# Kernel tuning notes

Hardware: AMD Instinct MI355X
Metric: run time of the kernel (lower is better)

Reference implementation:

```python
import jax, jax.numpy as jnp
import numpy as np

B, C, T, H, W = 8, 128, 16, 32, 32
M, N, CS = 64, 64, 64


def setup_inputs() -> dict:
    key = jax.random.key(0)
    ks = jax.random.split(key, 12)
    s = 0.02
    return {
        "input": jax.random.normal(ks[0], (B, C, T, H, W), dtype=jnp.float32),
        "condition": jax.random.normal(ks[1], (B, CS), dtype=jnp.float32),
        # 1x1x1 Conv3d weights collapse to (out, in) matrices
        "W_phi": jax.random.normal(ks[2], (M, C), dtype=jnp.float32) * s,
        "b_phi": jax.random.normal(ks[3], (M,), dtype=jnp.float32) * s,
        "W_theta": jax.random.normal(ks[4], (N, C), dtype=jnp.float32) * s,
        "b_theta": jax.random.normal(ks[5], (N,), dtype=jnp.float32) * s,
        "W_rho": jax.random.normal(ks[6], (N, C), dtype=jnp.float32) * s,
        "b_rho": jax.random.normal(ks[7], (N,), dtype=jnp.float32) * s,
        "W1": jax.random.normal(ks[8], (CS, CS), dtype=jnp.float32) * s,
        "b1": jax.random.normal(ks[9], (CS,), dtype=jnp.float32) * s,
        "W2": jax.random.normal(ks[10], (H * W, CS), dtype=jnp.float32) * s,
        "b2": jax.random.normal(ks[11], (H * W,), dtype=jnp.float32) * s,
    }


def _pointwise_conv3d(x, Wt, b):
    # Conv3d with kernel=1, stride=1 == channel mixing
    return jnp.einsum('bcthw,oc->bothw', x, Wt) + b[None, :, None, None, None]


def reference(input, condition, W_phi, b_phi, W_theta, b_theta, W_rho, b_rho, W1, b1, W2, b2):
    x = input.reshape(-1, C, T, H, W)
    cond = condition.reshape(x.shape[0], -1)
    A = _pointwise_conv3d(x, W_phi, b_phi)                       # (b,m,t,h,w)
    B0 = _pointwise_conv3d(x, W_theta, b_theta)                  # (b,n,t,h,w)
    Bm = jax.nn.softmax(B0.reshape(B0.shape[0], B0.shape[1], -1), axis=-1).reshape(B0.shape)
    # FC_Cond: Linear+ReLU, Linear+ReLU, then softmax over h*w
    h1 = jax.nn.relu(cond @ W1.T + b1)
    h2 = jax.nn.relu(h1 @ W2.T + b2)
    Cm = jax.nn.softmax(h2, axis=-1).reshape(-1, H, W)           # (b,h,w)
    BC = Bm * Cm[:, None, None, :, :]                            # (b,n,t,h,w)
    AB_T = jnp.einsum('bmthw,bnthw->bmn', A, BC)                 # (b,m,n)
    V = jax.nn.softmax(_pointwise_conv3d(x, W_rho, b_rho), axis=1)
    Z = jnp.einsum('bmn,bnthw->bmthw', AB_T, V)
    attn = jnp.transpose(Bm * V, (0, 1, 3, 4, 2))                # (b,n,h,w,t)
    return (Z, attn)
```

## Files before the change

### kernel.cpp

```cpp
#include <hip/hip_runtime.h>

#define CC 128
#define SB 16384

typedef _Float16 half4_t __attribute__((ext_vector_type(4)));
typedef _Float16 half8_t __attribute__((ext_vector_type(8)));
typedef float    f32x4  __attribute__((ext_vector_type(4)));

#define WH_OFF   0u
#define ABH_OFF  0u
#define BIAS_OFF 49152u
#define CM_OFF   50176u
#define SUME_OFF 82944u
#define XT_OFF   262144u
#define VT_OFF   33816576u

__global__ void k0_setup(const float* __restrict__ cond,
                         const float* __restrict__ W_phi, const float* __restrict__ b_phi,
                         const float* __restrict__ W_theta, const float* __restrict__ b_theta,
                         const float* __restrict__ W_rho, const float* __restrict__ b_rho,
                         const float* __restrict__ W1, const float* __restrict__ b1,
                         const float* __restrict__ W2, const float* __restrict__ b2,
                         char* __restrict__ wsc) {
  __shared__ float sc[64], sh1[64], red[256];
  int t = threadIdx.x, bid = blockIdx.x;
  if (bid < 8) {
    int b = bid;
    if (t < 64) sc[t] = cond[b*64 + t];
    __syncthreads();
    if (t < 64) {
      float acc = b1[t];
      for (int k = 0; k < 64; ++k) acc += sc[k] * W1[t*64 + k];
      sh1[t] = fmaxf(acc, 0.f);
    }
    __syncthreads();
    float ev[4]; float ps = 0.f;
    #pragma unroll
    for (int q = 0; q < 4; ++q) {
      int o = q*256 + t;
      float acc = b2[o];
      for (int k = 0; k < 64; ++k) acc += sh1[k] * W2[o*64 + k];
      ev[q] = __expf(fmaxf(acc, 0.f));
      ps += ev[q];
    }
    red[t] = ps; __syncthreads();
    for (int s = 128; s > 0; s >>= 1) { if (t < s) red[t] += red[t+s]; __syncthreads(); }
    float inv = 1.f / red[0];
    float* cm = (float*)(wsc + CM_OFF);
    #pragma unroll
    for (int q = 0; q < 4; ++q) cm[b*1024 + q*256 + t] = ev[q] * inv;
  } else {
    int r = bid - 8;
    _Float16* wh = (_Float16*)(wsc + WH_OFF);
    for (int i = r*256 + t; i < 24576; i += 2048) {
      int set = i >> 13, mk = i & 8191;
      const float* W = (set == 0) ? W_phi : (set == 1 ? W_theta : W_rho);
      wh[i] = (_Float16)W[mk];
    }
    if (r == 0 && t < 192) {
      float* bias = (float*)(wsc + BIAS_OFF);
      bias[t] = (t < 64) ? b_phi[t] : (t < 128 ? b_theta[t-64] : b_rho[t-128]);
    }
    if (r == 1) {
      float* se = (float*)(wsc + SUME_OFF);
      for (int i = t; i < 512; i += 256) se[i] = 0.f;
    }
  }
}

__global__ __launch_bounds__(256, 2) void kT_transpose(const float* __restrict__ x,
                                                       _Float16* __restrict__ xt) {
  __shared__ float Xs[128*133];
  int t = threadIdx.x, bid = blockIdx.x;
  int b = bid >> 7, chunk = bid & 127;
  int s0 = chunk * 128;
  const float* xb = x + (size_t)b*CC*SB + s0;
  #pragma unroll
  for (int r = 0; r < 16; ++r) {
    int fid = r*256 + t;
    int c = fid >> 5, s4 = (fid & 31) << 2;
    *(float4*)&Xs[c*133 + s4] = *(const float4*)(xb + (size_t)c*SB + s4);
  }
  __syncthreads();
  int c8 = t & 15, sl = t >> 4;
  _Float16* xo = xt + ((size_t)b*SB + s0)*128 + c8*8;
  #pragma unroll
  for (int it = 0; it < 8; ++it) {
    int s = it*16 + sl;
    half8_t h;
    #pragma unroll
    for (int i = 0; i < 8; ++i) h[i] = (_Float16)Xs[(c8*8 + i)*133 + s];
    *(half8_t*)(xo + (size_t)s*128) = h;
  }
}

__global__ __launch_bounds__(256, 2) void kC_main(
    const _Float16* __restrict__ xt, const _Float16* __restrict__ wh,
    const float* __restrict__ bias, const float* __restrict__ cm,
    float* __restrict__ sumE, _Float16* __restrict__ vt,
    char* __restrict__ ptb,
    float* __restrict__ part) {
  __shared__ _Float16 Xt_l[128*136];
  __shared__ _Float16 A_l[64*136];
  __shared__ _Float16 E_l[64*136];
  __shared__ float se_l[256];

  int t = threadIdx.x;
  int lane = t & 63, wv = t >> 6, ln = lane & 15, q = lane >> 4;
  int bid = blockIdx.x, b = bid >> 7, chunk = bid & 127;
  int s0 = chunk * 128;

  #pragma unroll
  for (int r = 0; r < 8; ++r) {
    int fid = r*256 + t;
    int s = fid >> 4, c16 = fid & 15;
    *(half8_t*)&Xt_l[s*136 + c16*8] =
        *(const half8_t*)(xt + ((size_t)b*SB + s0 + s)*128 + c16*8);
  }
  __syncthreads();

  half8_t bf[2][4];
  int myp = wv * 32;
  #pragma unroll
  for (int nt = 0; nt < 2; ++nt)
    #pragma unroll
    for (int kk = 0; kk < 4; ++kk)
      bf[nt][kk] = *(half8_t*)&Xt_l[(myp + nt*16 + ln)*136 + kk*32 + q*8];

  int gsl[2] = { s0 + myp + ln, s0 + myp + 16 + ln };
  float cmv[2] = { cm[b*1024 + (gsl[0] & 1023)], cm[b*1024 + (gsl[1] & 1023)] };

  half8_t af[4][4];
  f32x4 d[4][2];
  float ev[4][2][4];

  auto conv = [&](int setoff) {
    #pragma unroll
    for (int mt = 0; mt < 4; ++mt)
      #pragma unroll
      for (int kk = 0; kk < 4; ++kk)
        af[mt][kk] = *(const half8_t*)(wh + setoff + (mt*16 + ln)*128 + kk*32 + q*8);
    #pragma unroll
    for (int mt = 0; mt < 4; ++mt)
      #pragma unroll
      for (int nt = 0; nt < 2; ++nt)
        d[mt][nt] = (f32x4){0.f, 0.f, 0.f, 0.f};
    #pragma unroll
    for (int kk = 0; kk < 4; ++kk)
      #pragma unroll
      for (int mt = 0; mt < 4; ++mt)
        #pragma unroll
        for (int nt = 0; nt < 2; ++nt)
          d[mt][nt] = __builtin_amdgcn_mfma_f32_16x16x32_f16(af[mt][kk], bf[nt][kk],
                                                             d[mt][nt], 0, 0, 0);
  };

  conv(0);
  #pragma unroll
  for (int mt = 0; mt < 4; ++mt) {
    float bv[4]; *(float4*)bv = *(const float4*)(bias + mt*16 + q*4);
    #pragma unroll
    for (int nt = 0; nt < 2; ++nt)
      #pragma unroll
      for (int r = 0; r < 4; ++r)
        A_l[(mt*16 + q*4 + r)*136 + myp + nt*16 + ln] = (_Float16)(d[mt][nt][r] + bv[r]);
  }

  conv(8192);
  float sp[4][4];
  #pragma unroll
  for (int mt = 0; mt < 4; ++mt) {
    float bv[4]; *(float4*)bv = *(const float4*)(bias + 64 + mt*16 + q*4);
    #pragma unroll
    for (int r = 0; r < 4; ++r) {
      #pragma unroll
      for (int nt = 0; nt < 2; ++nt) {
        float e = __expf(d[mt][nt][r] + bv[r]);
        ev[mt][nt][r] = e;
        E_l[(mt*16 + q*4 + r)*136 + myp + nt*16 + ln] = (_Float16)(e * cmv[nt]);
      }
      sp[mt][r] = ev[mt][0][r] + ev[mt][1][r];
    }
  }
  #pragma unroll
  for (int mt = 0; mt < 4; ++mt)
    #pragma unroll
    for (int r = 0; r < 4; ++r) {
      float v = sp[mt][r];
      v += __shfl_xor(v, 1); v += __shfl_xor(v, 2);
      v += __shfl_xor(v, 4); v += __shfl_xor(v, 8);
      sp[mt][r] = v;
    }
  if (ln == 0) {
    #pragma unroll
    for (int mt = 0; mt < 4; ++mt)
      #pragma unroll
      for (int r = 0; r < 4; ++r)
        se_l[wv*64 + mt*16 + q*4 + r] = sp[mt][r];
  }

  conv(16384);
  #pragma unroll
  for (int mt = 0; mt < 4; ++mt) {
    float bv[4]; *(float4*)bv = *(const float4*)(bias + 128 + mt*16 + q*4);
    #pragma unroll
    for (int nt = 0; nt < 2; ++nt)
      #pragma unroll
      for (int r = 0; r < 4; ++r)
        d[mt][nt][r] = __expf(d[mt][nt][r] + bv[r]);
  }
  float cs[2] = {0.f, 0.f};
  #pragma unroll
  for (int mt = 0; mt < 4; ++mt)
    #pragma unroll
    for (int nt = 0; nt < 2; ++nt)
      #pragma unroll
      for (int r = 0; r < 4; ++r) cs[nt] += d[mt][nt][r];
  #pragma unroll
  for (int nt = 0; nt < 2; ++nt) {
    cs[nt] += __shfl_xor(cs[nt], 16);
    cs[nt] += __shfl_xor(cs[nt], 32);
    cs[nt] = 1.f / cs[nt];
  }
  #pragma unroll
  for (int nt = 0; nt < 2; ++nt) {
    size_t grow = (size_t)b*SB + gsl[nt];
    _Float16* vrow = vt + grow*64;
    char* prow = ptb + grow*256 + 128;
    #pragma unroll
    for (int mt = 0; mt < 4; ++mt) {
      half4_t hv, hp;
      #pragma unroll
      for (int r = 0; r < 4; ++r) {
        float vv = d[mt][nt][r] * cs[nt];
        hv[r] = (_Float16)vv;
        hp[r] = (_Float16)(vv * ev[mt][nt][r]);
      }
      *(half4_t*)(vrow + mt*16 + q*4) = hv;
      *(half4_t*)(prow + (size_t)(mt*16 + q*4)*2) = hp;
    }
  }
  __syncthreads();

  if (t < 64) {
    float ssum = se_l[t] + se_l[64+t] + se_l[128+t] + se_l[192+t];
    atomicAdd(&sumE[b*64 + t], ssum);
  }

  f32x4 dab[4];
  #pragma unroll
  for (int n2 = 0; n2 < 4; ++n2) dab[n2] = (f32x4){0.f, 0.f, 0.f, 0.f};
  #pragma unroll
  for (int kk = 0; kk < 4; ++kk) {
    half8_t aab = *(half8_t*)&A_l[(wv*16 + ln)*136 + kk*32 + q*8];
    #pragma unroll
    for (int n2 = 0; n2 < 4; ++n2) {
      half8_t bab = *(half8_t*)&E_l[(n2*16 + ln)*136 + kk*32 + q*8];
      dab[n2] = __builtin_amdgcn_mfma_f32_16x16x32_f16(aab, bab, dab[n2], 0, 0, 0);
    }
  }
  float* pp = part + (size_t)bid*4096;
  #pragma unroll
  for (int n2 = 0; n2 < 4; ++n2)
    #pragma unroll
    for (int r = 0; r < 4; ++r)
      pp[(wv*16 + q*4 + r)*64 + n2*16 + ln] = dab[n2][r];
}

__global__ void k2_reduce(const float* __restrict__ part, const float* __restrict__ sumE,
                          _Float16* __restrict__ abh) {
  int idx = blockIdx.x*256 + threadIdx.x;
  int b = idx >> 12, mn = idx & 4095, n = mn & 63;
  const float* p = part + (size_t)b*128*4096 + mn;
  float s = 0.f;
  #pragma unroll 4
  for (int k = 0; k < 128; ++k) s += p[(size_t)k*4096];
  abh[idx] = (_Float16)(s * (1024.f / sumE[b*64 + n]));
}

__global__ __launch_bounds__(256) void k3_z(const _Float16* __restrict__ abh,
                                            const _Float16* __restrict__ vt,
                                            float* __restrict__ zout) {
  __shared__ _Float16 Ah[64*72];
  int t = threadIdx.x;
  int lane = t & 63, wv = t >> 6, ln = lane & 15, q = lane >> 4;
  int bid = blockIdx.x, b = bid >> 6, chunk = bid & 63;
  int s0 = chunk * 256;
  #pragma unroll
  for (int r = 0; r < 2; ++r) {
    int fid = r*256 + t;
    int m = fid >> 3, n8 = fid & 7;
    *(half8_t*)&Ah[m*72 + n8*8] = *(const half8_t*)(abh + b*4096 + m*64 + n8*8);
  }
  __syncthreads();
  half8_t a8[4][2];
  #pragma unroll
  for (int mt = 0; mt < 4; ++mt)
    #pragma unroll
    for (int kk = 0; kk < 2; ++kk)
      a8[mt][kk] = *(half8_t*)&Ah[(mt*16 + ln)*72 + kk*32 + q*8];
  int sw = s0 + wv*64;
  #pragma unroll
  for (int nt = 0; nt < 4; ++nt) {
    int sb = sw + nt*16 + ln;
    const _Float16* vrow = vt + ((size_t)b*SB + sb)*64;
    half8_t b8[2];
    b8[0] = *(const half8_t*)(vrow + q*8);
    b8[1] = *(const half8_t*)(vrow + 32 + q*8);
    f32x4 dz[4];
    #pragma unroll
    for (int mt = 0; mt < 4; ++mt) dz[mt] = (f32x4){0.f, 0.f, 0.f, 0.f};
    #pragma unroll
    for (int kk = 0; kk < 2; ++kk)
      #pragma unroll
      for (int mt = 0; mt < 4; ++mt)
        dz[mt] = __builtin_amdgcn_mfma_f32_16x16x32_f16(a8[mt][kk], b8[kk], dz[mt], 0, 0, 0);
    #pragma unroll
    for (int mt = 0; mt < 4; ++mt)
      #pragma unroll
      for (int r = 0; r < 4; ++r)
        zout[((size_t)(b*64 + mt*16 + q*4 + r))*SB + sb] = dz[mt][r] * (1.f/1024.f);
  }
}

__global__ __launch_bounds__(256) void k4_attn(const char* __restrict__ ptb,
                                               const float* __restrict__ sumE,
                                               float* __restrict__ outA) {
  __shared__ _Float16 P_l[256*72];
  int t = threadIdx.x, bid = blockIdx.x;
  int b = bid >> 6, hw0 = (bid & 63) * 16;
  int st = t >> 4, h = t & 15;
  int s = st*1024 + hw0 + h;
  const char* prow = ptb + ((size_t)b*SB + s)*256 + 128;
  #pragma unroll
  for (int c8 = 0; c8 < 8; ++c8)
    *(half8_t*)&P_l[t*72 + c8*8] = *(const half8_t*)(prow + c8*16);
  __syncthreads();
  int n = t >> 2, oc = t & 3;
  float ri = 1.f / sumE[b*64 + n];
  float* orow = outA + 8388608 + (size_t)(b*64 + n)*SB + hw0*16;
  #pragma unroll
  for (int i = 0; i < 16; ++i) {
    int j = oc*64 + i*4;
    int hh = j >> 4, stb = j & 15;
    float w[4];
    #pragma unroll
    for (int r = 0; r < 4; ++r)
      w[r] = (float)P_l[((stb + r)*16 + hh)*72 + n] * ri;
    *(float4*)(orow + j) = *(float4*)w;
  }
}

extern "C" void kernel_launch(void* const* d_in, const int* in_sizes, int n_in,
                              void* d_out, int out_size, void* d_ws, size_t ws_size,
                              hipStream_t stream) {
  const float* input   = (const float*)d_in[0];
  const float* cond    = (const float*)d_in[1];
  const float* W_phi   = (const float*)d_in[2];
  const float* b_phi   = (const float*)d_in[3];
  const float* W_theta = (const float*)d_in[4];
  const float* b_theta = (const float*)d_in[5];
  const float* W_rho   = (const float*)d_in[6];
  const float* b_rho   = (const float*)d_in[7];
  const float* W1      = (const float*)d_in[8];
  const float* b1      = (const float*)d_in[9];
  const float* W2      = (const float*)d_in[10];
  const float* b2      = (const float*)d_in[11];
  char* wsc = (char*)d_ws;
  float* out = (float*)d_out;

  const _Float16* wh = (const _Float16*)(wsc + WH_OFF);
  _Float16* abh  = (_Float16*)(wsc + ABH_OFF);
  const float* bias = (const float*)(wsc + BIAS_OFF);
  const float* cmp  = (const float*)(wsc + CM_OFF);
  float* sumE  = (float*)(wsc + SUME_OFF);
  _Float16* xt = (_Float16*)(wsc + XT_OFF);
  _Float16* vt = (_Float16*)(wsc + VT_OFF);
  float* part  = out + 8388608;

  hipLaunchKernelGGL(k0_setup, dim3(16), dim3(256), 0, stream,
                     cond, W_phi, b_phi, W_theta, b_theta, W_rho, b_rho,
                     W1, b1, W2, b2, wsc);
  hipLaunchKernelGGL(kT_transpose, dim3(1024), dim3(256), 0, stream, input, xt);
  hipLaunchKernelGGL(kC_main, dim3(1024), dim3(256), 0, stream,
                     xt, wh, bias, cmp, sumE, vt, (char*)(wsc + XT_OFF), part);
  hipLaunchKernelGGL(k2_reduce, dim3(128), dim3(256), 0, stream, part, sumE, abh);
  hipLaunchKernelGGL(k3_z, dim3(512), dim3(256), 0, stream, abh, vt, out);
  hipLaunchKernelGGL(k4_attn, dim3(512), dim3(256), 0, stream,
                     (const char*)(wsc + XT_OFF), sumE, out);
}
```

Baseline: 227.1 us.

## Fuse input transpose into main kernel and merge Z/attn kernels

Removes the separate fp32-to-fp16 transpose kernel. The main kernel now loads the channel-major input directly, converts it to fp16 in shared memory, and gathers the MFMA B fragments with strided LDS reads. Shared memory is aliased and the occupancy hint is raised to 4 blocks per CU. The P buffer is compacted to 128 bytes per row, k3 and k4 are merged into one launch split by block index, and k2 uses 128-thread blocks. This saves a full global round trip of the input and two launches, at the cost of scalar strided LDS gathers and possible bank conflicts.

```diff
diff --git a/kernel.cpp b/kernel.cpp
--- a/kernel.cpp
+++ b/kernel.cpp
@@ -3,6 +3,7 @@
 #define CC 128
 #define SB 16384
 
+typedef _Float16 half2_t __attribute__((ext_vector_type(2)));
 typedef _Float16 half4_t __attribute__((ext_vector_type(4)));
 typedef _Float16 half8_t __attribute__((ext_vector_type(8)));
 typedef float    f32x4  __attribute__((ext_vector_type(4)));
@@ -12,7 +13,7 @@
 #define BIAS_OFF 49152u
 #define CM_OFF   50176u
 #define SUME_OFF 82944u
-#define XT_OFF   262144u
+#define PT_OFF   262144u
 #define VT_OFF   33816576u
 
 __global__ void k0_setup(const float* __restrict__ cond,
@@ -68,67 +69,53 @@
   }
 }
 
-__global__ __launch_bounds__(256, 2) void kT_transpose(const float* __restrict__ x,
-                                                       _Float16* __restrict__ xt) {
-  __shared__ float Xs[128*133];
-  int t = threadIdx.x, bid = blockIdx.x;
-  int b = bid >> 7, chunk = bid & 127;
-  int s0 = chunk * 128;
-  const float* xb = x + (size_t)b*CC*SB + s0;
-  #pragma unroll
-  for (int r = 0; r < 16; ++r) {
-    int fid = r*256 + t;
-    int c = fid >> 5, s4 = (fid & 31) << 2;
-    *(float4*)&Xs[c*133 + s4] = *(const float4*)(xb + (size_t)c*SB + s4);
-  }
-  __syncthreads();
-  int c8 = t & 15, sl = t >> 4;
-  _Float16* xo = xt + ((size_t)b*SB + s0)*128 + c8*8;
-  #pragma unroll
-  for (int it = 0; it < 8; ++it) {
-    int s = it*16 + sl;
-    half8_t h;
-    #pragma unroll
-    for (int i = 0; i < 8; ++i) h[i] = (_Float16)Xs[(c8*8 + i)*133 + s];
-    *(half8_t*)(xo + (size_t)s*128) = h;
-  }
-}
-
-__global__ __launch_bounds__(256, 2) void kC_main(
-    const _Float16* __restrict__ xt, const _Float16* __restrict__ wh,
+__global__ __launch_bounds__(256, 4) void kC_main(
+    const float* __restrict__ x, const _Float16* __restrict__ wh,
     const float* __restrict__ bias, const float* __restrict__ cm,
     float* __restrict__ sumE, _Float16* __restrict__ vt,
     char* __restrict__ ptb,
     float* __restrict__ part) {
-  __shared__ _Float16 Xt_l[128*136];
-  __shared__ _Float16 A_l[64*136];
-  __shared__ _Float16 E_l[64*136];
+  __shared__ char smem[35328];
   __shared__ float se_l[256];
+  _Float16* Xh  = (_Float16*)smem;
+  _Float16* A_l = (_Float16*)smem;
+  _Float16* E_l = (_Float16*)(smem + 17408);
 
   int t = threadIdx.x;
   int lane = t & 63, wv = t >> 6, ln = lane & 15, q = lane >> 4;
   int bid = blockIdx.x, b = bid >> 7, chunk = bid & 127;
   int s0 = chunk * 128;
 
-  #pragma unroll
-  for (int r = 0; r < 8; ++r) {
+  const float* xb = x + (size_t)b*CC*SB + s0;
+  #pragma unroll
+  for (int r = 0; r < 16; ++r) {
     int fid = r*256 + t;
-    int s = fid >> 4, c16 = fid & 15;
-    *(half8_t*)&Xt_l[s*136 + c16*8] =
-        *(const half8_t*)(xt + ((size_t)b*SB + s0 + s)*128 + c16*8);
+    int c = fid >> 5, s4 = (fid & 31) << 2;
+    float4 v = *(const float4*)(xb + (size_t)c*SB + s4);
+    half2_t p0 = { (_Float16)v.x, (_Float16)v.y };
+    half2_t p1 = { (_Float16)v.z, (_Float16)v.w };
+    *(half2_t*)&Xh[c*138 + s4]     = p0;
+    *(half2_t*)&Xh[c*138 + s4 + 2] = p1;
   }
   __syncthreads();
 
+  int myp = wv * 32;
   half8_t bf[2][4];
-  int myp = wv * 32;
-  #pragma unroll
-  for (int nt = 0; nt < 2; ++nt)
-    #pragma unroll
-    for (int kk = 0; kk < 4; ++kk)
-      bf[nt][kk] = *(half8_t*)&Xt_l[(myp + nt*16 + ln)*136 + kk*32 + q*8];
+  #pragma unroll
+  for (int nt = 0; nt < 2; ++nt) {
+    int s = myp + nt*16 + ln;
+    #pragma unroll
+    for (int kk = 0; kk < 4; ++kk) {
+      half8_t h;
+      #pragma unroll
+      for (int j = 0; j < 8; ++j) h[j] = Xh[(kk*32 + q*8 + j)*138 + s];
+      bf[nt][kk] = h;
+    }
+  }
 
   int gsl[2] = { s0 + myp + ln, s0 + myp + 16 + ln };
   float cmv[2] = { cm[b*1024 + (gsl[0] & 1023)], cm[b*1024 + (gsl[1] & 1023)] };
+  __syncthreads();
 
   half8_t af[4][4];
   f32x4 d[4][2];
@@ -226,7 +213,7 @@
   for (int nt = 0; nt < 2; ++nt) {
     size_t grow = (size_t)b*SB + gsl[nt];
     _Float16* vrow = vt + grow*64;
-    char* prow = ptb + grow*256 + 128;
+    char* prow = ptb + grow*128;
     #pragma unroll
     for (int mt = 0; mt < 4; ++mt) {
       half4_t hv, hp;
@@ -269,85 +256,86 @@
 
 __global__ void k2_reduce(const float* __restrict__ part, const float* __restrict__ sumE,
                           _Float16* __restrict__ abh) {
-  int idx = blockIdx.x*256 + threadIdx.x;
+  int idx = blockIdx.x*128 + threadIdx.x;
   int b = idx >> 12, mn = idx & 4095, n = mn & 63;
   const float* p = part + (size_t)b*128*4096 + mn;
   float s = 0.f;
-  #pragma unroll 4
+  #pragma unroll 8
   for (int k = 0; k < 128; ++k) s += p[(size_t)k*4096];
   abh[idx] = (_Float16)(s * (1024.f / sumE[b*64 + n]));
 }
 
-__global__ __launch_bounds__(256) void k3_z(const _Float16* __restrict__ abh,
-                                            const _Float16* __restrict__ vt,
-                                            float* __restrict__ zout) {
-  __shared__ _Float16 Ah[64*72];
+__global__ __launch_bounds__(256) void k34(const _Float16* __restrict__ abh,
+                                           const _Float16* __restrict__ vt,
+                                           const char* __restrict__ ptb,
+                                           const float* __restrict__ sumE,
+                                           float* __restrict__ out) {
+  __shared__ _Float16 sm[256*72];
   int t = threadIdx.x;
-  int lane = t & 63, wv = t >> 6, ln = lane & 15, q = lane >> 4;
-  int bid = blockIdx.x, b = bid >> 6, chunk = bid & 63;
-  int s0 = chunk * 256;
-  #pragma unroll
-  for (int r = 0; r < 2; ++r) {
-    int fid = r*256 + t;
-    int m = fid >> 3, n8 = fid & 7;
-    *(half8_t*)&Ah[m*72 + n8*8] = *(const half8_t*)(abh + b*4096 + m*64 + n8*8);
-  }
-  __syncthreads();
-  half8_t a8[4][2];
-  #pragma unroll
-  for (int mt = 0; mt < 4; ++mt)
-    #pragma unroll
-    for (int kk = 0; kk < 2; ++kk)
-      a8[mt][kk] = *(half8_t*)&Ah[(mt*16 + ln)*72 + kk*32 + q*8];
-  int sw = s0 + wv*64;
-  #pragma unroll
-  for (int nt = 0; nt < 4; ++nt) {
-    int sb = sw + nt*16 + ln;
-    const _Float16* vrow = vt + ((size_t)b*SB + sb)*64;
-    half8_t b8[2];
-    b8[0] = *(const half8_t*)(vrow + q*8);
-    b8[1] = *(const half8_t*)(vrow + 32 + q*8);
-    f32x4 dz[4];
-    #pragma unroll
-    for (int mt = 0; mt < 4; ++mt) dz[mt] = (f32x4){0.f, 0.f, 0.f, 0.f};
-    #pragma unroll
-    for (int kk = 0; kk < 2; ++kk)
+  if (blockIdx.x < 512) {
+    _Float16* Ah = sm;
+    int lane = t & 63, wv = t >> 6, ln = lane & 15, q = lane >> 4;
+    int bid = blockIdx.x, b = bid >> 6, chunk = bid & 63;
+    int s0 = chunk * 256;
+    #pragma unroll
+    for (int r = 0; r < 2; ++r) {
+      int fid = r*256 + t;
+      int m = fid >> 3, n8 = fid & 7;
+      *(half8_t*)&Ah[m*72 + n8*8] = *(const half8_t*)(abh + b*4096 + m*64 + n8*8);
+    }
+    __syncthreads();
+    half8_t a8[4][2];
+    #pragma unroll
+    for (int mt = 0; mt < 4; ++mt)
+      #pragma unroll
+      for (int kk = 0; kk < 2; ++kk)
+        a8[mt][kk] = *(half8_t*)&Ah[(mt*16 + ln)*72 + kk*32 + q*8];
+    int sw = s0 + wv*64;
+    #pragma unroll
+    for (int nt = 0; nt < 4; ++nt) {
+      int sb = sw + nt*16 + ln;
+      const _Float16* vrow = vt + ((size_t)b*SB + sb)*64;
+      half8_t b8[2];
+      b8[0] = *(const half8_t*)(vrow + q*8);
+      b8[1] = *(const half8_t*)(vrow + 32 + q*8);
+      f32x4 dz[4];
+      #pragma unroll
+      for (int mt = 0; mt < 4; ++mt) dz[mt] = (f32x4){0.f, 0.f, 0.f, 0.f};
+      #pragma unroll
+      for (int kk = 0; kk < 2; ++kk)
+        #pragma unroll
+        for (int mt = 0; mt < 4; ++mt)
+          dz[mt] = __builtin_amdgcn_mfma_f32_16x16x32_f16(a8[mt][kk], b8[kk], dz[mt], 0, 0, 0);
       #pragma unroll
       for (int mt = 0; mt < 4; ++mt)
-        dz[mt] = __builtin_amdgcn_mfma_f32_16x16x32_f16(a8[mt][kk], b8[kk], dz[mt], 0, 0, 0);
-    #pragma unroll
-    for (int mt = 0; mt < 4; ++mt)
+        #pragma unroll
+        for (int r = 0; r < 4; ++r)
+          out[((size_t)(b*64 + mt*16 + q*4 + r))*SB + sb] = dz[mt][r] * (1.f/1024.f);
+    }
+  } else {
+    _Float16* P_l = sm;
+    int bid = blockIdx.x - 512;
+    int b = bid >> 6, hw0 = (bid & 63) * 16;
+    int st = t >> 4, h = t & 15;
+    int s = st*1024 + hw0 + h;
+    const char* prow = ptb + ((size_t)b*SB + s)*128;
+    #pragma unroll
+    for (int c8 = 0; c8 < 8; ++c8)
+      *(half8_t*)&P_l[t*72 + c8*8] = *(const half8_t*)(prow + c8*16);
+    __syncthreads();
+    int n = t >> 2, oc = t & 3;
+    float ri = 1.f / sumE[b*64 + n];
+    float* orow = out + 8388608 + (size_t)(b*64 + n)*SB + hw0*16;
+    #pragma unroll
+    for (int i = 0; i < 16; ++i) {
+      int j = oc*64 + i*4;
+      int hh = j >> 4, stb = j & 15;
+      float w[4];
       #pragma unroll
       for (int r = 0; r < 4; ++r)
-        zout[((size_t)(b*64 + mt*16 + q*4 + r))*SB + sb] = dz[mt][r] * (1.f/1024.f);
-  }
-}
-
-__global__ __launch_bounds__(256) void k4_attn(const char* __restrict__ ptb,
-                                               const float* __restrict__ sumE,
-                                               float* __restrict__ outA) {
-  __shared__ _Float16 P_l[256*72];
-  int t = threadIdx.x, bid = blockIdx.x;
-  int b = bid >> 6, hw0 = (bid & 63) * 16;
-  int st = t >> 4, h = t & 15;
-  int s = st*1024 + hw0 + h;
-  const char* prow = ptb + ((size_t)b*SB + s)*256 + 128;
-  #pragma unroll
-  for (int c8 = 0; c8 < 8; ++c8)
-    *(half8_t*)&P_l[t*72 + c8*8] = *(const half8_t*)(prow + c8*16);
-  __syncthreads();
-  int n = t >> 2, oc = t & 3;
-  float ri = 1.f / sumE[b*64 + n];
-  float* orow = outA + 8388608 + (size_t)(b*64 + n)*SB + hw0*16;
-  #pragma unroll
-  for (int i = 0; i < 16; ++i) {
-    int j = oc*64 + i*4;
-    int hh = j >> 4, stb = j & 15;
-    float w[4];
-    #pragma unroll
-    for (int r = 0; r < 4; ++r)
-      w[r] = (float)P_l[((stb + r)*16 + hh)*72 + n] * ri;
-    *(float4*)(orow + j) = *(float4*)w;
+        w[r] = (float)P_l[((stb + r)*16 + hh)*72 + n] * ri;
+      *(float4*)(orow + j) = *(float4*)w;
+    }
   }
 }
 
@@ -374,18 +362,15 @@
   const float* bias = (const float*)(wsc + BIAS_OFF);
   const float* cmp  = (const float*)(wsc + CM_OFF);
   float* sumE  = (float*)(wsc + SUME_OFF);
-  _Float16* xt = (_Float16*)(wsc + XT_OFF);
   _Float16* vt = (_Float16*)(wsc + VT_OFF);
   float* part  = out + 8388608;
 
   hipLaunchKernelGGL(k0_setup, dim3(16), dim3(256), 0, stream,
                      cond, W_phi, b_phi, W_theta, b_theta, W_rho, b_rho,
                      W1, b1, W2, b2, wsc);
-  hipLaunchKernelGGL(kT_transpose, dim3(1024), dim3(256), 0, stream, input, xt);
   hipLaunchKernelGGL(kC_main, dim3(1024), dim3(256), 0, stream,
-                     xt, wh, bias, cmp, sumE, vt, (char*)(wsc + XT_OFF), part);
-  hipLaunchKernelGGL(k2_reduce, dim3(128), dim3(256), 0, stream, part, sumE, abh);
-  hipLaunchKernelGGL(k3_z, dim3(512), dim3(256), 0, stream, abh, vt, out);
-  hipLaunchKernelGGL(k4_attn, dim3(512), dim3(256), 0, stream,
-                     (const char*)(wsc + XT_OFF), sumE, out);
-}
+                     input, wh, bias, cmp, sumE, vt, (char*)(wsc + PT_OFF), part);
+  hipLaunchKernelGGL(k2_reduce, dim3(256), dim3(128), 0, stream, part, sumE, abh);
+  hipLaunchKernelGGL(k34, dim3(1024), dim3(256), 0, stream,
+                     abh, vt, (const char*)(wsc + PT_OFF), sumE, out);
+}
```

After: 211.4 us. 1.07x faster.
